# Performance work log

Hardware: AMD Instinct MI355X
Metric: run time of the kernel (lower is better)

The kernel has to match this reference:

```python
import jax, jax.numpy as jnp
import numpy as np


def log_g(x):
    # log of g(x) = x+0.5 for x>=0, sigmoid(x) for x<0, computed stably
    return jnp.where(x >= 0, jnp.log(jax.nn.relu(x) + 0.5), -jax.nn.softplus(-x))


def setup_inputs() -> dict:
    key = jax.random.key(0)
    k1, k2 = jax.random.split(key)
    B, S, D = 4, 4096, 1024
    x = jax.random.normal(k1, (B, S, D), dtype=jnp.float32)
    W = jax.random.normal(k2, (D, 3 * D), dtype=jnp.float32) * (1.0 / np.sqrt(D))
    return {"x": x, "W": W}


def reference(x, W):
    # fused gate projection: [B,S,D] @ [D,3D] -> f_gate, i_gate, hidden
    gates = jnp.einsum('bsd,de->bse', x, W)
    f_gate, i_gate, hidden = jnp.split(gates, 3, axis=-1)

    # log-space normalized gates: log_f = log(sig(f)/(sig(f)+sig(i))) etc.
    diff = jax.nn.softplus(-f_gate) - jax.nn.softplus(-i_gate)
    log_f = -jax.nn.softplus(diff)
    log_i = -jax.nn.softplus(-diff)
    log_tilde_h = log_g(hidden)

    log_values = log_i + log_tilde_h
    # parallel scan in log space over seq axis (axis=1)
    a_star = jnp.cumsum(log_f, axis=1)
    log_h0_plus_b_star = jax.lax.cumlogsumexp(log_values - a_star, axis=1)
    h = jnp.exp(a_star + log_h0_plus_b_star)  # [B,S,D]
    return h  # to_out is Identity for expansion_factor == 1.0
```

## Files before the change

### kernel.cpp

```cpp
#include <hip/hip_runtime.h>
#include <hip/hip_fp16.h>
#include <cstdint>

typedef _Float16 half8  __attribute__((ext_vector_type(8)));
typedef _Float16 half4v __attribute__((ext_vector_type(4)));
typedef _Float16 half2v __attribute__((ext_vector_type(2)));
typedef float    floatx4 __attribute__((ext_vector_type(4)));

constexpr int Bb = 4, Ss = 4096, Dd = 1024;
constexpr int Mdim = Bb * Ss;
constexpr int Ndim = 3 * Dd;
constexpr int Kdim = Dd;
constexpr int CH = 256, LCH = Ss / CH;

__device__ __forceinline__ void gload_lds16(const void* g, void* l) {
  __builtin_amdgcn_global_load_lds(
      (const __attribute__((address_space(1))) uint32_t*)g,
      (__attribute__((address_space(3))) uint32_t*)l, 16, 0, 0);
}

__device__ __forceinline__ void gate_fv(float fg, float ig, float hg,
                                        float& fw, float& v) {
  float ef = __expf(fminf(-fg, 40.f));
  float ei = __expf(fminf(-ig, 40.f));
  float r  = __builtin_amdgcn_rcpf(2.f + ef + ei);
  fw = (1.f + ei) * r;
  float iw = (1.f + ef) * r;
  float g  = hg >= 0.f ? hg + 0.5f
                       : __builtin_amdgcn_rcpf(1.f + __expf(fminf(-hg, 40.f)));
  v = iw * g;
}

__global__ __launch_bounds__(256) void cvt_k(const float* __restrict__ X,
                                             _Float16* __restrict__ X16,
                                             const float* __restrict__ W,
                                             _Float16* __restrict__ WT) {
  __shared__ float tile[32][33];
  int bid = blockIdx.x;
  if (bid < 2048) {
    const int n4 = Mdim * Kdim / 4;
    for (int i = bid * 256 + threadIdx.x; i < n4; i += 2048 * 256) {
      float4 v = ((const float4*)X)[i];
      half4v o = {(_Float16)v.x, (_Float16)v.y, (_Float16)v.z, (_Float16)v.w};
      ((half4v*)X16)[i] = o;
    }
  } else {
    int b2 = bid - 2048;
    int tx = threadIdx.x & 31, ty = threadIdx.x >> 5;
    int n0 = (b2 % 96) * 32, k0 = (b2 / 96) * 32;
#pragma unroll
    for (int j = 0; j < 4; ++j) {
      int k = ty + j * 8;
      tile[k][tx] = W[(int64_t)(k0 + k) * Ndim + n0 + tx];
    }
    __syncthreads();
#pragma unroll
    for (int j = 0; j < 4; ++j) {
      int nl = ty + j * 8;
      int n = n0 + nl;
      int g = n >> 10, d = n & 1023;
      int p = (d >> 6) * 192 + g * 64 + (d & 63);
      WT[(int64_t)p * Kdim + k0 + tx] = (_Float16)tile[tx][nl];
    }
  }
}

constexpr int GBM = 128, GBN = 192, GBK = 64;
constexpr int NT = Kdim / GBK;
constexpr int LBUF = 40960;

__global__ __launch_bounds__(512, 4) void gemm8_k(const _Float16* __restrict__ A,
                                                  const _Float16* __restrict__ BT,
                                                  _Float16* __restrict__ fv,
                                                  float* __restrict__ Fc,
                                                  float* __restrict__ Hc) {
  extern __shared__ char lds[];
  const int tid = threadIdx.x;
  const int wid = tid >> 6, lane = tid & 63;
  const int wm = wid >> 2, wn = wid & 3;
  const int l15 = lane & 15, lq = lane >> 4;

  int wg = blockIdx.x;
  wg = (wg & 7) * 256 + (wg >> 3);
  const int m0 = (wg >> 4) * GBM;
  const int d0 = (wg & 15) * 64;

  int aO[4];
#pragma unroll
  for (int mi = 0; mi < 4; ++mi) {
    int r = wm * 64 + mi * 16 + l15;
    aO[mi] = r * 128 + ((lq ^ (r & 7)) << 4);
  }
  const int rB = wn * 16 + l15;
  const int bO = rB * 128 + ((lq ^ (rB & 7)) << 4);

  const int srr = (wid << 3) + (lane >> 3);
  const int ss = lane & 7;
  const _Float16* Abase = A + (size_t)m0 * Kdim;
  const _Float16* Bbase = BT + (size_t)(wg & 15) * 192 * Kdim;

  auto stage = [&](const _Float16* gsrc, int ldsBase, int nr) {
#pragma unroll
    for (int round = 0; round < 3; ++round) {
      if (round >= nr) break;
      int r = (round << 6) + srr;
      int c = ss ^ (r & 7);
      gload_lds16(gsrc + (size_t)r * Kdim + (c << 3),
                  lds + ldsBase + (round << 13) + (wid << 10));
    }
  };

  floatx4 acc[4][3] = {};

  stage(Abase, 0, 2);
  stage(Bbase, 16384, 3);
  stage(Abase + 64, LBUF, 2);
  stage(Bbase + 64, LBUF + 16384, 3);
  asm volatile("s_waitcnt vmcnt(5)" ::: "memory");
  __builtin_amdgcn_s_barrier();

  for (int kt = 0; kt < NT; ++kt) {
    const int cur = (kt & 1) * LBUF;

    half8 a[4][2], b[3][2];
#pragma unroll
    for (int mi = 0; mi < 4; ++mi)
#pragma unroll
      for (int ks = 0; ks < 2; ++ks)
        a[mi][ks] = *(const half8*)(lds + cur + (aO[mi] ^ (ks << 6)));
#pragma unroll
    for (int g = 0; g < 3; ++g)
#pragma unroll
      for (int ks = 0; ks < 2; ++ks)
        b[g][ks] = *(const half8*)(lds + cur + 16384 + (g << 13) + (bO ^ (ks << 6)));

    __builtin_amdgcn_s_setprio(1);
#pragma unroll
    for (int ks = 0; ks < 2; ++ks)
#pragma unroll
      for (int mi = 0; mi < 2; ++mi)
#pragma unroll
        for (int g = 0; g < 3; ++g)
          acc[mi][g] = __builtin_amdgcn_mfma_f32_16x16x32_f16(
              a[mi][ks], b[g][ks], acc[mi][g], 0, 0, 0);
    __builtin_amdgcn_s_setprio(0);

    __builtin_amdgcn_s_barrier();
    if (kt + 2 < NT) {
      const _Float16* Ak = Abase + (kt + 2) * GBK;
      const _Float16* Bk = Bbase + (kt + 2) * GBK;
      stage(Ak, cur, 2);
      stage(Bk, cur + 16384, 3);
    }

    __builtin_amdgcn_s_setprio(1);
#pragma unroll
    for (int ks = 0; ks < 2; ++ks)
#pragma unroll
      for (int mi = 2; mi < 4; ++mi)
#pragma unroll
        for (int g = 0; g < 3; ++g)
          acc[mi][g] = __builtin_amdgcn_mfma_f32_16x16x32_f16(
              a[mi][ks], b[g][ks], acc[mi][g], 0, 0, 0);
    __builtin_amdgcn_s_setprio(0);

    if (kt < NT - 2) {
      asm volatile("s_waitcnt vmcnt(5)" ::: "memory");
      __builtin_amdgcn_s_barrier();
    } else if (kt == NT - 2) {
      asm volatile("s_waitcnt vmcnt(0)" ::: "memory");
      __builtin_amdgcn_s_barrier();
    }
  }

  const int dcol = d0 + wn * 16 + l15;
#pragma unroll
  for (int mf = 0; mf < 4; ++mf) {
    int row0 = m0 + wm * 64 + mf * 16;
    float Fl = 1.f, Hl = 0.f;
#pragma unroll
    for (int r = 0; r < 4; ++r) {
      float fw, v;
      gate_fv(acc[mf][0][r], acc[mf][1][r], acc[mf][2][r], fw, v);
      half2v o = {(_Float16)fw, (_Float16)v};
      *(half2v*)(fv + ((size_t)(row0 + (lq << 2) + r) * Dd + dcol) * 2) = o;
      float fr = (float)o[0], vr = (float)o[1];
      Hl = fmaf(fr, Hl, vr);
      Fl *= fr;
    }
    float Fg = 1.f, Hg = 0.f;
#pragma unroll
    for (int j = 0; j < 4; ++j) {
      float Fj = __shfl(Fl, j * 16 + l15);
      float Hj = __shfl(Hl, j * 16 + l15);
      Hg = fmaf(Fj, Hg, Hj);
      Fg *= Fj;
    }
    if (lq == 0) {
      int bb = row0 >> 12, s0 = row0 & (Ss - 1);
      int co = (bb * CH + (s0 >> 4)) * Dd + dcol;
      Fc[co] = Fg;
      Hc[co] = Hg;
    }
  }
}

__global__ __launch_bounds__(256) void scan2_k(const float* __restrict__ Fc,
                                               const float* __restrict__ Hc,
                                               float* __restrict__ Carry) {
  int idx = blockIdx.x * 256 + threadIdx.x;
  int b = idx >> 10, d = idx & (Dd - 1);
  float carry = 0.f;
#pragma unroll 8
  for (int c = 0; c < CH; ++c) {
    int co = (b * CH + c) * Dd + d;
    Carry[co] = carry;
    carry = fmaf(Fc[co], carry, Hc[co]);
  }
}

__global__ __launch_bounds__(256) void scan3_k(const _Float16* __restrict__ fv,
                                               const float* __restrict__ Carry,
                                               float* __restrict__ Out) {
  int d = threadIdx.x * 4;
  int c = blockIdx.y, b = blockIdx.z;
  int64_t m0 = (int64_t)(b * Ss + c * LCH);
  const _Float16* p = fv + (m0 * Dd + d) * 2;
  float* o = Out + m0 * Dd + d;
  int co = (b * CH + c) * Dd + d;
  floatx4 hv = *(const floatx4*)(Carry + co);
  float h[4] = {hv[0], hv[1], hv[2], hv[3]};
#pragma unroll 4
  for (int s = 0; s < LCH; ++s) {
    half8 q = *(const half8*)p;
#pragma unroll
    for (int j = 0; j < 4; ++j)
      h[j] = fmaf((float)q[2 * j], h[j], (float)q[2 * j + 1]);
    *(floatx4*)o = *(floatx4*)h;
    p += Dd * 2;
    o += Dd;
  }
}

extern "C" void kernel_launch(void* const* d_in, const int* in_sizes, int n_in,
                              void* d_out, int out_size, void* d_ws, size_t ws_size,
                              hipStream_t stream) {
  const float* x = (const float*)d_in[0];
  const float* W = (const float*)d_in[1];
  float* out = (float*)d_out;

  char* ws = (char*)d_ws;
  size_t off = 0;
  auto alloc = [&](size_t bytes) {
    char* p = ws + off;
    off += (bytes + 255) & ~size_t(255);
    return p;
  };
  _Float16* fv     = (_Float16*)alloc((size_t)Mdim * Dd * 2 * 2);
  float* Fc        = (float*)alloc((size_t)Bb * CH * Dd * 4);
  float* Hc        = (float*)alloc((size_t)Bb * CH * Dd * 4);
  float* Carry     = (float*)alloc((size_t)Bb * CH * Dd * 4);
  _Float16* x16    = (_Float16*)alloc((size_t)Mdim * Kdim * 2);
  _Float16* w16t   = (_Float16*)alloc((size_t)Ndim * Kdim * 2);
  if (off > ws_size) return;

  cvt_k<<<5120, 256, 0, stream>>>(x, x16, W, w16t);
  gemm8_k<<<dim3((Mdim / GBM) * (Dd / 64)), 512, 81920, stream>>>(x16, w16t, fv, Fc, Hc);
  scan2_k<<<(Bb * Dd) / 256, 256, 0, stream>>>(Fc, Hc, Carry);
  scan3_k<<<dim3(1, CH, Bb), 256, 0, stream>>>(fv, Carry, out);
}
```

Baseline: 176.3 us.

## Fuse fp32-to-fp16 conversion of X into GEMM A-tile loading

Removes the separate pass that converts X to fp16 in global memory. The GEMM now loads fp32 X into registers one tile ahead, converts to fp16, and writes the swizzled result to LDS, while B keeps the async global-to-LDS path. This saves a full write and re-read of the fp16 copy of X, but the GEMM must now read twice as many bytes for A (about 16 times over, once per N-block). It also uses more registers and changes the wait-counter pipeline.

```diff
diff --git a/kernel.cpp b/kernel.cpp
--- a/kernel.cpp
+++ b/kernel.cpp
@@ -31,37 +31,25 @@
   v = iw * g;
 }
 
-__global__ __launch_bounds__(256) void cvt_k(const float* __restrict__ X,
-                                             _Float16* __restrict__ X16,
-                                             const float* __restrict__ W,
-                                             _Float16* __restrict__ WT) {
+__global__ __launch_bounds__(256) void cvt_w_k(const float* __restrict__ W,
+                                               _Float16* __restrict__ WT) {
   __shared__ float tile[32][33];
-  int bid = blockIdx.x;
-  if (bid < 2048) {
-    const int n4 = Mdim * Kdim / 4;
-    for (int i = bid * 256 + threadIdx.x; i < n4; i += 2048 * 256) {
-      float4 v = ((const float4*)X)[i];
-      half4v o = {(_Float16)v.x, (_Float16)v.y, (_Float16)v.z, (_Float16)v.w};
-      ((half4v*)X16)[i] = o;
-    }
-  } else {
-    int b2 = bid - 2048;
-    int tx = threadIdx.x & 31, ty = threadIdx.x >> 5;
-    int n0 = (b2 % 96) * 32, k0 = (b2 / 96) * 32;
-#pragma unroll
-    for (int j = 0; j < 4; ++j) {
-      int k = ty + j * 8;
-      tile[k][tx] = W[(int64_t)(k0 + k) * Ndim + n0 + tx];
-    }
-    __syncthreads();
-#pragma unroll
-    for (int j = 0; j < 4; ++j) {
-      int nl = ty + j * 8;
-      int n = n0 + nl;
-      int g = n >> 10, d = n & 1023;
-      int p = (d >> 6) * 192 + g * 64 + (d & 63);
-      WT[(int64_t)p * Kdim + k0 + tx] = (_Float16)tile[tx][nl];
-    }
+  int b2 = blockIdx.x;
+  int tx = threadIdx.x & 31, ty = threadIdx.x >> 5;
+  int n0 = (b2 % 96) * 32, k0 = (b2 / 96) * 32;
+#pragma unroll
+  for (int j = 0; j < 4; ++j) {
+    int k = ty + j * 8;
+    tile[k][tx] = W[(int64_t)(k0 + k) * Ndim + n0 + tx];
+  }
+  __syncthreads();
+#pragma unroll
+  for (int j = 0; j < 4; ++j) {
+    int nl = ty + j * 8;
+    int n = n0 + nl;
+    int g = n >> 10, d = n & 1023;
+    int p = (d >> 6) * 192 + g * 64 + (d & 63);
+    WT[(int64_t)p * Kdim + k0 + tx] = (_Float16)tile[tx][nl];
   }
 }
 
@@ -69,7 +57,7 @@
 constexpr int NT = Kdim / GBK;
 constexpr int LBUF = 40960;
 
-__global__ __launch_bounds__(512, 4) void gemm8_k(const _Float16* __restrict__ A,
+__global__ __launch_bounds__(512, 4) void gemm8_k(const float* __restrict__ X,
                                                   const _Float16* __restrict__ BT,
                                                   _Float16* __restrict__ fv,
                                                   float* __restrict__ Fc,
@@ -96,13 +84,12 @@
 
   const int srr = (wid << 3) + (lane >> 3);
   const int ss = lane & 7;
-  const _Float16* Abase = A + (size_t)m0 * Kdim;
+  const float* Xbase = X + (size_t)m0 * Kdim;
   const _Float16* Bbase = BT + (size_t)(wg & 15) * 192 * Kdim;
 
-  auto stage = [&](const _Float16* gsrc, int ldsBase, int nr) {
+  auto stageB = [&](const _Float16* gsrc, int ldsBase) {
 #pragma unroll
     for (int round = 0; round < 3; ++round) {
-      if (round >= nr) break;
       int r = (round << 6) + srr;
       int c = ss ^ (r & 7);
       gload_lds16(gsrc + (size_t)r * Kdim + (c << 3),
@@ -110,13 +97,37 @@
     }
   };
 
+  float4 ar[2][2];
+  auto fillA = [&](int kt) {
+#pragma unroll
+    for (int round = 0; round < 2; ++round) {
+      int r = (round << 6) + srr;
+      int c = ss ^ (r & 7);
+      const float4* s =
+          (const float4*)(Xbase + (size_t)r * Kdim + kt * GBK + (c << 3));
+      ar[round][0] = s[0];
+      ar[round][1] = s[1];
+    }
+  };
+  auto writeA = [&](int ldsBase) {
+#pragma unroll
+    for (int round = 0; round < 2; ++round) {
+      half8 o = {(_Float16)ar[round][0].x, (_Float16)ar[round][0].y,
+                 (_Float16)ar[round][0].z, (_Float16)ar[round][0].w,
+                 (_Float16)ar[round][1].x, (_Float16)ar[round][1].y,
+                 (_Float16)ar[round][1].z, (_Float16)ar[round][1].w};
+      *(half8*)(lds + ldsBase + (round << 13) + (wid << 10) + (lane << 4)) = o;
+    }
+  };
+
   floatx4 acc[4][3] = {};
 
-  stage(Abase, 0, 2);
-  stage(Bbase, 16384, 3);
-  stage(Abase + 64, LBUF, 2);
-  stage(Bbase + 64, LBUF + 16384, 3);
-  asm volatile("s_waitcnt vmcnt(5)" ::: "memory");
+  fillA(0); writeA(0);
+  fillA(1); writeA(LBUF);
+  stageB(Bbase, 16384);
+  stageB(Bbase + 64, LBUF + 16384);
+  fillA(2);
+  asm volatile("s_waitcnt vmcnt(7) lgkmcnt(0)" ::: "memory");
   __builtin_amdgcn_s_barrier();
 
   for (int kt = 0; kt < NT; ++kt) {
@@ -147,11 +158,10 @@
 
     __builtin_amdgcn_s_barrier();
     if (kt + 2 < NT) {
-      const _Float16* Ak = Abase + (kt + 2) * GBK;
-      const _Float16* Bk = Bbase + (kt + 2) * GBK;
-      stage(Ak, cur, 2);
-      stage(Bk, cur + 16384, 3);
-    }
+      writeA(cur);
+      stageB(Bbase + (kt + 2) * GBK, cur + 16384);
+    }
+    if (kt + 3 < NT) fillA(kt + 3);
 
     __builtin_amdgcn_s_setprio(1);
 #pragma unroll
@@ -165,10 +175,10 @@
     __builtin_amdgcn_s_setprio(0);
 
     if (kt < NT - 2) {
-      asm volatile("s_waitcnt vmcnt(5)" ::: "memory");
+      asm volatile("s_waitcnt lgkmcnt(0)" ::: "memory");
       __builtin_amdgcn_s_barrier();
     } else if (kt == NT - 2) {
-      asm volatile("s_waitcnt vmcnt(0)" ::: "memory");
+      asm volatile("s_waitcnt vmcnt(0) lgkmcnt(0)" ::: "memory");
       __builtin_amdgcn_s_barrier();
     }
   }
@@ -260,12 +270,11 @@
   float* Fc        = (float*)alloc((size_t)Bb * CH * Dd * 4);
   float* Hc        = (float*)alloc((size_t)Bb * CH * Dd * 4);
   float* Carry     = (float*)alloc((size_t)Bb * CH * Dd * 4);
-  _Float16* x16    = (_Float16*)alloc((size_t)Mdim * Kdim * 2);
   _Float16* w16t   = (_Float16*)alloc((size_t)Ndim * Kdim * 2);
   if (off > ws_size) return;
 
-  cvt_k<<<5120, 256, 0, stream>>>(x, x16, W, w16t);
-  gemm8_k<<<dim3((Mdim / GBM) * (Dd / 64)), 512, 81920, stream>>>(x16, w16t, fv, Fc, Hc);
+  cvt_w_k<<<96 * 32, 256, 0, stream>>>(W, w16t);
+  gemm8_k<<<dim3((Mdim / GBM) * (Dd / 64)), 512, 81920, stream>>>(x, w16t, fv, Fc, Hc);
   scan2_k<<<(Bb * Dd) / 256, 256, 0, stream>>>(Fc, Hc, Carry);
   scan3_k<<<dim3(1, CH, Bb), 256, 0, stream>>>(fv, Carry, out);
 }
```

Result: slower. 234.4 us (+33.0%).

## Load GEMM B operand directly from global into registers, shrink LDS

Applied to the files above, without the earlier changes.

The gate-projection GEMM now reads the W tile straight from global memory into registers for each wave, instead of staging it through LDS. Only the A tile is still double-buffered in LDS, which cuts the dynamic LDS allocation from 80KB to 32KB so more workgroups can be resident per CU. The end-of-iteration waitcnt and barrier are also removed. That saves sync cost but leaves no cross-wave guarantee that the A-tile DMA writes are complete before they are read. B data is now fetched redundantly by the four M-waves through the cache hierarchy rather than shared through LDS.

```diff
diff --git a/kernel.cpp b/kernel.cpp
--- a/kernel.cpp
+++ b/kernel.cpp
@@ -67,7 +67,7 @@
 
 constexpr int GBM = 128, GBN = 192, GBK = 64;
 constexpr int NT = Kdim / GBK;
-constexpr int LBUF = 40960;
+constexpr int LBUF = 16384;
 
 __global__ __launch_bounds__(512, 4) void gemm8_k(const _Float16* __restrict__ A,
                                                   const _Float16* __restrict__ BT,
@@ -91,18 +91,14 @@
     int r = wm * 64 + mi * 16 + l15;
     aO[mi] = r * 128 + ((lq ^ (r & 7)) << 4);
   }
-  const int rB = wn * 16 + l15;
-  const int bO = rB * 128 + ((lq ^ (rB & 7)) << 4);
 
   const int srr = (wid << 3) + (lane >> 3);
   const int ss = lane & 7;
   const _Float16* Abase = A + (size_t)m0 * Kdim;
-  const _Float16* Bbase = BT + (size_t)(wg & 15) * 192 * Kdim;
-
-  auto stage = [&](const _Float16* gsrc, int ldsBase, int nr) {
-#pragma unroll
-    for (int round = 0; round < 3; ++round) {
-      if (round >= nr) break;
+
+  auto stageA = [&](const _Float16* gsrc, int ldsBase) {
+#pragma unroll
+    for (int round = 0; round < 2; ++round) {
       int r = (round << 6) + srr;
       int c = ss ^ (r & 7);
       gload_lds16(gsrc + (size_t)r * Kdim + (c << 3),
@@ -110,29 +106,35 @@
     }
   };
 
+  const _Float16* Bpanel = BT + (size_t)(wg & 15) * 192 * Kdim;
+  const _Float16* pB[3];
+#pragma unroll
+  for (int g = 0; g < 3; ++g)
+    pB[g] = Bpanel + (size_t)(g * 64 + wn * 16 + l15) * Kdim + lq * 8;
+
   floatx4 acc[4][3] = {};
 
-  stage(Abase, 0, 2);
-  stage(Bbase, 16384, 3);
-  stage(Abase + 64, LBUF, 2);
-  stage(Bbase + 64, LBUF + 16384, 3);
-  asm volatile("s_waitcnt vmcnt(5)" ::: "memory");
+  stageA(Abase, 0);
+  stageA(Abase + GBK, LBUF);
+  asm volatile("s_waitcnt vmcnt(2)" ::: "memory");
   __builtin_amdgcn_s_barrier();
 
   for (int kt = 0; kt < NT; ++kt) {
     const int cur = (kt & 1) * LBUF;
 
-    half8 a[4][2], b[3][2];
+    half8 b[3][2];
+#pragma unroll
+    for (int g = 0; g < 3; ++g)
+#pragma unroll
+      for (int ks = 0; ks < 2; ++ks)
+        b[g][ks] = *(const half8*)(pB[g] + kt * GBK + (ks << 5));
+
+    half8 a[4][2];
 #pragma unroll
     for (int mi = 0; mi < 4; ++mi)
 #pragma unroll
       for (int ks = 0; ks < 2; ++ks)
         a[mi][ks] = *(const half8*)(lds + cur + (aO[mi] ^ (ks << 6)));
-#pragma unroll
-    for (int g = 0; g < 3; ++g)
-#pragma unroll
-      for (int ks = 0; ks < 2; ++ks)
-        b[g][ks] = *(const half8*)(lds + cur + 16384 + (g << 13) + (bO ^ (ks << 6)));
 
     __builtin_amdgcn_s_setprio(1);
 #pragma unroll
@@ -146,12 +148,7 @@
     __builtin_amdgcn_s_setprio(0);
 
     __builtin_amdgcn_s_barrier();
-    if (kt + 2 < NT) {
-      const _Float16* Ak = Abase + (kt + 2) * GBK;
-      const _Float16* Bk = Bbase + (kt + 2) * GBK;
-      stage(Ak, cur, 2);
-      stage(Bk, cur + 16384, 3);
-    }
+    if (kt + 2 < NT) stageA(Abase + (kt + 2) * GBK, cur);
 
     __builtin_amdgcn_s_setprio(1);
 #pragma unroll
@@ -163,14 +160,6 @@
           acc[mi][g] = __builtin_amdgcn_mfma_f32_16x16x32_f16(
               a[mi][ks], b[g][ks], acc[mi][g], 0, 0, 0);
     __builtin_amdgcn_s_setprio(0);
-
-    if (kt < NT - 2) {
-      asm volatile("s_waitcnt vmcnt(5)" ::: "memory");
-      __builtin_amdgcn_s_barrier();
-    } else if (kt == NT - 2) {
-      asm volatile("s_waitcnt vmcnt(0)" ::: "memory");
-      __builtin_amdgcn_s_barrier();
-    }
   }
 
   const int dcol = d0 + wn * 16 + l15;
@@ -265,7 +254,7 @@
   if (off > ws_size) return;
 
   cvt_k<<<5120, 256, 0, stream>>>(x, x16, W, w16t);
-  gemm8_k<<<dim3((Mdim / GBM) * (Dd / 64)), 512, 81920, stream>>>(x16, w16t, fv, Fc, Hc);
+  gemm8_k<<<dim3((Mdim / GBM) * (Dd / 64)), 512, 32768, stream>>>(x16, w16t, fv, Fc, Hc);
   scan2_k<<<(Bb * Dd) / 256, 256, 0, stream>>>(Fc, Hc, Carry);
   scan3_k<<<dim3(1, CH, Bb), 256, 0, stream>>>(fv, Carry, out);
 }
```

After: 268.1 us. +52.1%, slower.

## Pack four consecutive rows of fv per column into one 16-byte store

Applied to the files above, without the earlier changes.

The GEMM epilogue now collects the (f, v) pairs for four consecutive rows in one half8 and writes them as a single 16-byte store, in a layout grouped by 4-row blocks and column. The scan3 kernel is changed to match: one thread per column, 16-byte loads each covering four timesteps, and a grid four times larger in x. This swaps many scattered 4-byte stores in the GEMM for wide ones. In exchange, scan3 output writes become single-float per thread (still coalesced across threads), and each thread handles one column instead of four.

```diff
diff --git a/kernel.cpp b/kernel.cpp
--- a/kernel.cpp
+++ b/kernel.cpp
@@ -12,6 +12,7 @@
 constexpr int Ndim = 3 * Dd;
 constexpr int Kdim = Dd;
 constexpr int CH = 256, LCH = Ss / CH;
+
 
 __device__ __forceinline__ void gload_lds16(const void* g, void* l) {
   __builtin_amdgcn_global_load_lds(
@@ -178,16 +179,18 @@
   for (int mf = 0; mf < 4; ++mf) {
     int row0 = m0 + wm * 64 + mf * 16;
     float Fl = 1.f, Hl = 0.f;
+    half8 o;
 #pragma unroll
     for (int r = 0; r < 4; ++r) {
       float fw, v;
       gate_fv(acc[mf][0][r], acc[mf][1][r], acc[mf][2][r], fw, v);
-      half2v o = {(_Float16)fw, (_Float16)v};
-      *(half2v*)(fv + ((size_t)(row0 + (lq << 2) + r) * Dd + dcol) * 2) = o;
-      float fr = (float)o[0], vr = (float)o[1];
+      o[2 * r] = (_Float16)fw;
+      o[2 * r + 1] = (_Float16)v;
+      float fr = (float)o[2 * r], vr = (float)o[2 * r + 1];
       Hl = fmaf(fr, Hl, vr);
       Fl *= fr;
     }
+    *(half8*)(fv + ((size_t)((row0 >> 2) + lq) * Dd + dcol) * 8) = o;
     float Fg = 1.f, Hg = 0.f;
 #pragma unroll
     for (int j = 0; j < 4; ++j) {
@@ -222,23 +225,20 @@
 __global__ __launch_bounds__(256) void scan3_k(const _Float16* __restrict__ fv,
                                                const float* __restrict__ Carry,
                                                float* __restrict__ Out) {
-  int d = threadIdx.x * 4;
+  int d = blockIdx.x * 256 + threadIdx.x;
   int c = blockIdx.y, b = blockIdx.z;
-  int64_t m0 = (int64_t)(b * Ss + c * LCH);
-  const _Float16* p = fv + (m0 * Dd + d) * 2;
-  float* o = Out + m0 * Dd + d;
-  int co = (b * CH + c) * Dd + d;
-  floatx4 hv = *(const floatx4*)(Carry + co);
-  float h[4] = {hv[0], hv[1], hv[2], hv[3]};
-#pragma unroll 4
-  for (int s = 0; s < LCH; ++s) {
-    half8 q = *(const half8*)p;
-#pragma unroll
-    for (int j = 0; j < 4; ++j)
-      h[j] = fmaf((float)q[2 * j], h[j], (float)q[2 * j + 1]);
-    *(floatx4*)o = *(floatx4*)h;
-    p += Dd * 2;
-    o += Dd;
+  int row0 = b * Ss + c * LCH;
+  const _Float16* p = fv + ((size_t)(row0 >> 2) * Dd + d) * 8;
+  float* o = Out + (size_t)row0 * Dd + d;
+  float h = Carry[(b * CH + c) * Dd + d];
+#pragma unroll
+  for (int j = 0; j < 4; ++j) {
+    half8 q = *(const half8*)(p + (size_t)j * Dd * 8);
+#pragma unroll
+    for (int r = 0; r < 4; ++r) {
+      h = fmaf((float)q[2 * r], h, (float)q[2 * r + 1]);
+      o[(size_t)(j * 4 + r) * Dd] = h;
+    }
   }
 }
 
@@ -267,5 +267,5 @@
   cvt_k<<<5120, 256, 0, stream>>>(x, x16, W, w16t);
   gemm8_k<<<dim3((Mdim / GBM) * (Dd / 64)), 512, 81920, stream>>>(x16, w16t, fv, Fc, Hc);
   scan2_k<<<(Bb * Dd) / 256, 256, 0, stream>>>(Fc, Hc, Carry);
-  scan3_k<<<dim3(1, CH, Bb), 256, 0, stream>>>(fv, Carry, out);
-}
+  scan3_k<<<dim3(4, CH, Bb), 256, 0, stream>>>(fv, Carry, out);
+}
```

Result: no change. 174.5 us (-1.0%).
